# Kernel tuning notes

Measured on AMD Instinct MI355X. Metric: run time of the kernel, lower is better.

## Reference

```python
import jax, jax.numpy as jnp
import numpy as np

HID = 2048
H = 16
D_NOPE = 128
D_ROPE = 64
HEAD_DIM = D_NOPE + D_ROPE  # 192
V_DIM = 128
KV_RANK = 512
Q_RANK = 1536
THETA = 10000.0
EPS = 1e-6
B, S = 2, 2048


def _rope_cos_sin(seq_len):
    # half-dim frequencies: cos/sin have shape (seq_len, D_ROPE//2)
    inv_freq = 1.0 / (THETA ** (jnp.arange(0, D_ROPE, 2, dtype=jnp.float32) / D_ROPE))
    freqs = jnp.arange(seq_len, dtype=jnp.float32)[:, None] * inv_freq[None, :]
    return jnp.cos(freqs), jnp.sin(freqs)


def _apply_rope(x, cos, sin):
    # x: (..., D_ROPE); cos/sin broadcastable to (..., D_ROPE//2)
    half = x.shape[-1] // 2
    x1, x2 = x[..., :half], x[..., half:]
    return jnp.concatenate([x1 * cos - x2 * sin, x2 * cos + x1 * sin], axis=-1)


def _rmsnorm(x, w):
    ms = jnp.mean(jnp.square(x), axis=-1, keepdims=True)
    return x * jax.lax.rsqrt(ms + EPS) * w


def setup_inputs() -> dict:
    key = jax.random.key(0)
    ks = jax.random.split(key, 7)
    std = 0.02
    return {
        "x": jax.random.normal(ks[0], (B, S, HID), dtype=jnp.float32),
        "w_q_down": jax.random.normal(ks[1], (HID, Q_RANK), dtype=jnp.float32) * std,
        "w_q_up": jax.random.normal(ks[2], (Q_RANK, H * HEAD_DIM), dtype=jnp.float32) * std,
        "w_kv_down": jax.random.normal(ks[3], (HID, KV_RANK + D_ROPE), dtype=jnp.float32) * std,
        "kv_norm_w": jnp.ones((KV_RANK,), dtype=jnp.float32),
        "w_kv_up": jax.random.normal(ks[4], (KV_RANK, H * (D_NOPE + V_DIM)), dtype=jnp.float32) * std,
        "w_out": jax.random.normal(ks[5], (H * V_DIM, HID), dtype=jnp.float32) * std,
    }


def reference(x, w_q_down, w_q_up, w_kv_down, kv_norm_w, w_kv_up, w_out):
    b, s, _ = x.shape
    scale = 1.0 / np.sqrt(HEAD_DIM)

    # query: low-rank down then up, split into nope/rope parts
    q = (x @ w_q_down) @ w_q_up                      # (b, s, H*HEAD_DIM)
    q = q.reshape(b, s, H, HEAD_DIM)
    q_nope, q_rope = q[..., :D_NOPE], q[..., D_NOPE:]

    # KV: compressed latent + rope key component
    kv_full = x @ w_kv_down                          # (b, s, KV_RANK + D_ROPE)
    kv_c, k_rope = kv_full[..., :KV_RANK], kv_full[..., KV_RANK:]
    kv_c = _rmsnorm(kv_c, kv_norm_w)

    kv_exp = (kv_c @ w_kv_up).reshape(b, s, H, D_NOPE + V_DIM)
    k_nope, v = kv_exp[..., :D_NOPE], kv_exp[..., D_NOPE:]

    # RoPE (no past_kv -> q_offset = 0, kv_len = s)
    cos, sin = _rope_cos_sin(s)                      # (s, D_ROPE//2)
    cos4, sin4 = cos[None, :, None, :], sin[None, :, None, :]
    q_rope = _apply_rope(q_rope, cos4, sin4)         # (b, s, H, D_ROPE)
    k_rope = _apply_rope(k_rope, cos[None], sin[None])  # (b, s, D_ROPE)

    k_rope_h = jnp.broadcast_to(k_rope[:, :, None, :], (b, s, H, D_ROPE))
    k = jnp.concatenate([k_nope, k_rope_h], axis=-1)     # (b, s, H, HEAD_DIM)
    q_full = jnp.concatenate([q_nope, q_rope], axis=-1)  # (b, s, H, HEAD_DIM)

    # causal SDPA
    scores = jnp.einsum("bqhd,bkhd->bhqk", q_full, k) * scale
    causal = jnp.tril(jnp.ones((s, s), dtype=bool))
    scores = jnp.where(causal[None, None], scores, jnp.finfo(scores.dtype).min)
    attn = jax.nn.softmax(scores, axis=-1)
    out = jnp.einsum("bhqk,bkhd->bqhd", attn, v)     # (b, s, H, V_DIM)
    out = out.reshape(b, s, H * V_DIM)
    return out @ w_out
```

## Files before the change

### kernel.cpp

```cpp
#include <hip/hip_runtime.h>
#include <hip/hip_bf16.h>
#include <math.h>

#define HID    2048
#define NH     16
#define D_NOPE 128
#define D_ROPE 64
#define HD     192
#define V_DIM  128
#define KV_RANK 512
#define Q_RANK  1536
#define BATCH  2
#define SEQ    2048
#define ROWS   (BATCH*SEQ)

typedef __attribute__((ext_vector_type(8))) short short8;
typedef __attribute__((ext_vector_type(4))) float f32x4;

__device__ __forceinline__ unsigned short f2bf(float x) {
    unsigned int u = __float_as_uint(x);
    unsigned int r = (u + 0x7fffu + ((u >> 16) & 1u)) >> 16;
    return (unsigned short)r;
}
__device__ __forceinline__ float bf2f(unsigned short u) {
    return __uint_as_float((unsigned int)u << 16);
}

typedef const __attribute__((address_space(1))) unsigned int gu32;
typedef __attribute__((address_space(3))) unsigned int lu32;
__device__ __forceinline__ void gl_lds16(const void* g, void* l) {
    __builtin_amdgcn_global_load_lds((gu32*)g, (lu32*)l, 16, 0, 0);
}

template<int CTRL>
__device__ __forceinline__ float dpp_mv(float x) {
    return __int_as_float(__builtin_amdgcn_update_dpp(
        __float_as_int(x), __float_as_int(x), CTRL, 0xF, 0xF, true));
}
__device__ __forceinline__ float rowmax16(float x) {
    x = fmaxf(x, dpp_mv<0xB1>(x));
    x = fmaxf(x, dpp_mv<0x4E>(x));
    x = fmaxf(x, dpp_mv<0x141>(x));
    x = fmaxf(x, dpp_mv<0x140>(x));
    return x;
}

__global__ void rope_table_kernel(float* __restrict__ table) {
    int idx = blockIdx.x * 256 + threadIdx.x;
    int pos = idx >> 6, u = idx & 63;
    int i = u & 31;
    float invf = expf((float)i * (-9.210340371976184f / 32.0f));
    float ang = (float)pos * invf;
    table[idx] = (u < 32) ? cosf(ang) : sinf(ang);
}

__global__ __launch_bounds__(256) void convert_bf16_kernel(
    const float* __restrict__ src, unsigned short* __restrict__ dst)
{
    size_t i = (size_t)(blockIdx.x * 256 + threadIdx.x) * 4;
    float4 v = *(const float4*)(src + i);
    ushort4 u;
    u.x = f2bf(v.x); u.y = f2bf(v.y); u.z = f2bf(v.z); u.w = f2bf(v.w);
    *(ushort4*)(dst + i) = u;
}

__global__ __launch_bounds__(256) void transpose_bf16_kernel(
    const float* __restrict__ src, unsigned short* __restrict__ dst, int K, int N)
{
    __shared__ float T[64][65];
    const int n0 = blockIdx.x * 64, k0 = blockIdx.y * 64;
    const int t = threadIdx.x;
    const int c4 = t & 15, r = t >> 4;
    #pragma unroll
    for (int i = 0; i < 4; i++) {
        int row = r + i * 16;
        float4 v = *(const float4*)(src + (size_t)(k0 + row) * N + n0 + c4 * 4);
        T[row][c4*4+0] = v.x; T[row][c4*4+1] = v.y;
        T[row][c4*4+2] = v.z; T[row][c4*4+3] = v.w;
    }
    __syncthreads();
    #pragma unroll
    for (int i = 0; i < 4; i++) {
        int nrow = r + i * 16;
        ushort4 u;
        u.x = f2bf(T[c4*4+0][nrow]); u.y = f2bf(T[c4*4+1][nrow]);
        u.z = f2bf(T[c4*4+2][nrow]); u.w = f2bf(T[c4*4+3][nrow]);
        *(ushort4*)(dst + (size_t)(n0 + nrow) * K + k0 + c4 * 4) = u;
    }
}

template<int BN, bool OUT_BF16>
__global__ __launch_bounds__(256) void bgemm_kernel(
    const unsigned short* __restrict__ A,
    const unsigned short* __restrict__ Bt,
    void* __restrict__ Cv,
    int M, int N, int K)
{
    constexpr int NT = BN / 32;
    constexpr int NSLAB = 8 + BN / 16;
    const int tid  = threadIdx.x;
    const int w    = tid >> 6;
    const int lane = tid & 63;
    const int n16  = lane & 15, quad = lane >> 4;
    const int m0 = blockIdx.y * 128;
    const int n0 = blockIdx.x * BN;
    const int moff = (w & 1) * 64;
    const int noff = (w >> 1) * (NT * 16);

    __shared__ unsigned short As[128 * 32];
    __shared__ unsigned short Bs[BN * 32];

    const unsigned short* gp[4];
    unsigned short* lp[4];
    int ns = 0;
    const int rl = lane >> 2, sc = lane & 3;
    for (int s = w; s < NSLAB; s += 4) {
        int kc = sc ^ (((s * 16 + rl) >> 1) & 3);
        if (s < 8) {
            gp[ns] = A + (size_t)(m0 + s * 16 + rl) * K + kc * 8;
            lp[ns] = As + s * 512;
        } else {
            int sb = s - 8;
            gp[ns] = Bt + (size_t)(n0 + sb * 16 + rl) * K + kc * 8;
            lp[ns] = Bs + sb * 512;
        }
        ns++;
    }

    const int swz = (quad ^ ((n16 >> 1) & 3)) * 8;
    int aoff[4], boff[NT];
    #pragma unroll
    for (int mt = 0; mt < 4; mt++) aoff[mt] = (moff + mt * 16 + n16) * 32 + swz;
    #pragma unroll
    for (int nt = 0; nt < NT; nt++) boff[nt] = (noff + nt * 16 + n16) * 32 + swz;

    f32x4 acc[4][NT];
    #pragma unroll
    for (int mt = 0; mt < 4; mt++)
        #pragma unroll
        for (int nt = 0; nt < NT; nt++) acc[mt][nt] = (f32x4){0.f, 0.f, 0.f, 0.f};

    for (int k0 = 0; k0 < K; k0 += 32) {
        #pragma unroll
        for (int j = 0; j < 4; j++) if (j < ns) gl_lds16(gp[j], lp[j]);
        #pragma unroll
        for (int j = 0; j < 4; j++) if (j < ns) gp[j] += 32;
        __syncthreads();

        short8 af[4], bfr[NT];
        #pragma unroll
        for (int mt = 0; mt < 4; mt++) af[mt] = *(const short8*)(As + aoff[mt]);
        #pragma unroll
        for (int nt = 0; nt < NT; nt++) bfr[nt] = *(const short8*)(Bs + boff[nt]);
        #pragma unroll
        for (int mt = 0; mt < 4; mt++)
            #pragma unroll
            for (int nt = 0; nt < NT; nt++)
                acc[mt][nt] = __builtin_amdgcn_mfma_f32_16x16x32_bf16(
                    af[mt], bfr[nt], acc[mt][nt], 0, 0, 0);
        __syncthreads();
    }

    #pragma unroll
    for (int mt = 0; mt < 4; mt++)
        #pragma unroll
        for (int nt = 0; nt < NT; nt++)
            #pragma unroll
            for (int r = 0; r < 4; r++) {
                size_t idx = (size_t)(m0 + moff + mt * 16 + quad * 4 + r) * N
                           + n0 + noff + nt * 16 + n16;
                if (OUT_BF16) ((unsigned short*)Cv)[idx] = f2bf(acc[mt][nt][r]);
                else          ((float*)Cv)[idx] = acc[mt][nt][r];
            }
}

__global__ __launch_bounds__(256) void kv_norm_rope_kernel(
    const float* __restrict__ kv_full,
    const float* __restrict__ w,
    const float* __restrict__ table,
    unsigned short* __restrict__ kv_cb,
    unsigned short* __restrict__ k_rope_b)
{
    const int row = blockIdx.x;
    const int tid = threadIdx.x;
    const float* src = kv_full + (size_t)row * 576;
    float v0 = src[tid], v1 = src[tid + 256];
    float ss = v0*v0 + v1*v1;
    #pragma unroll
    for (int off = 32; off > 0; off >>= 1) ss += __shfl_down(ss, off);
    __shared__ float red[4];
    __shared__ float msh;
    if ((tid & 63) == 0) red[tid >> 6] = ss;
    __syncthreads();
    if (tid == 0) msh = (red[0] + red[1] + red[2] + red[3]) * (1.0f / 512.0f);
    __syncthreads();
    float f = rsqrtf(msh + 1e-6f);
    kv_cb[(size_t)row * 512 + tid]       = f2bf(v0 * f * w[tid]);
    kv_cb[(size_t)row * 512 + tid + 256] = f2bf(v1 * f * w[tid + 256]);
    if (tid < 32) {
        int pos = row & (SEQ - 1);
        float c = table[pos*64 + tid], s = table[pos*64 + 32 + tid];
        float x1 = src[512 + tid], x2 = src[512 + 32 + tid];
        k_rope_b[(size_t)row * 64 + tid]      = f2bf(x1*c - x2*s);
        k_rope_b[(size_t)row * 64 + 32 + tid] = f2bf(x2*c + x1*s);
    }
}

__global__ __launch_bounds__(256) void q_rope_b_kernel(
    unsigned short* __restrict__ qb16, const float* __restrict__ table)
{
    int g = blockIdx.x * 8 + (threadIdx.x >> 5);
    int i = threadIdx.x & 31;
    int row = g >> 4, h = g & 15;
    size_t base = (size_t)row * (NH*HD) + h * HD + D_NOPE;
    int pos = row & (SEQ - 1);
    float c = table[pos*64 + i], s = table[pos*64 + 32 + i];
    float x1 = bf2f(qb16[base + i]), x2 = bf2f(qb16[base + 32 + i]);
    qb16[base + i]      = f2bf(x1*c - x2*s);
    qb16[base + 32 + i] = f2bf(x2*c + x1*s);
}

__global__ __launch_bounds__(256) void pack_vt_kernel(
    const unsigned short* __restrict__ kv_exp_b, unsigned short* __restrict__ Vmat)
{
    const int st = blockIdx.x;
    const int h  = blockIdx.y;
    const int b  = blockIdx.z;
    const int tid = threadIdx.x;
    const int s0 = st * 64;
    __shared__ float T[64][129];

    #pragma unroll
    for (int t = 0; t < 8; t++) {
        int idx = tid + t * 256;
        int tokr = idx >> 5, c4 = idx & 31;
        ushort4 u = *(const ushort4*)(kv_exp_b +
            ((size_t)(b*SEQ) + s0 + tokr) * 4096 + h*256 + 128 + c4*4);
        T[tokr][c4*4+0] = bf2f(u.x); T[tokr][c4*4+1] = bf2f(u.y);
        T[tokr][c4*4+2] = bf2f(u.z); T[tokr][c4*4+3] = bf2f(u.w);
    }
    __syncthreads();

    int d = tid >> 1, sh = (tid & 1) * 32;
    unsigned short* op = Vmat + ((size_t)((b*NH + h) * V_DIM + d)) * SEQ + s0 + sh;
    #pragma unroll
    for (int j = 0; j < 32; j += 2) {
        ushort2 u;
        u.x = f2bf(T[sh + j][d]);
        u.y = f2bf(T[sh + j + 1][d]);
        *(ushort2*)(op + j) = u;
    }
}

__global__ __launch_bounds__(256, 3) void flash_mfma_kernel(
    const unsigned short* __restrict__ qb16,
    const unsigned short* __restrict__ kv_exp_b,
    const unsigned short* __restrict__ k_rope_b,
    const unsigned short* __restrict__ Vmat,
    unsigned short* __restrict__ attnb)
{
    const int bid  = blockIdx.x;
    const int xcd  = bid & 7, slot = bid >> 3;
    const int grp  = xcd + 8 * (slot >> 5);
    const int qb   = 31 - (slot & 31);
    const int h    = grp & 15, b = grp >> 4;
    const int tid  = threadIdx.x;
    const int w    = tid >> 6;
    const int lane = tid & 63;
    const int n16  = lane & 15;
    const int quad = lane >> 4;

    const int q0 = qb * 64 + w * 16;
    const char* kNopeB = (const char*)(kv_exp_b + (size_t)b * SEQ * 4096 + h * 256);
    const char* kRopeB = (const char*)(k_rope_b + (size_t)b * SEQ * 64);
    const char* vByte  = (const char*)(Vmat + (size_t)(b*NH + h) * V_DIM * SEQ);

    __shared__ unsigned short Ks[2][6144];
    __shared__ unsigned short Vs[2][4096];
    __shared__ unsigned short Plds[4][16][40];

    const char* gK[2]; int lK[2];
    #pragma unroll
    for (int t = 0; t < 2; t++) {
        int idx = t * 256 + tid;
        int kc = idx >> 7, key = (idx >> 2) & 31, sc = idx & 3;
        int scs = sc ^ ((key >> 1) & 3);
        gK[t] = kNopeB + (size_t)key * 8192 + kc * 64 + scs * 16;
        lK[t] = idx * 16;
    }
    const char* gR; int lR;
    {
        int kc = tid >> 7, key = (tid >> 2) & 31, sc = tid & 3;
        int scs = sc ^ ((key >> 1) & 3);
        gR = kRopeB + (size_t)key * 128 + kc * 64 + scs * 16;
        lR = (512 + tid) * 16;
    }
    const char* gV[2]; int lV[2];
    #pragma unroll
    for (int t = 0; t < 2; t++) {
        int idx = t * 256 + tid;
        int d = idx >> 2, sc = idx & 3;
        int scs = sc ^ ((d >> 1) & 3);
        gV[t] = vByte + (size_t)d * (SEQ * 2) + scs * 16;
        lV[t] = idx * 16;
    }

    auto stage = [&](int kt, int bufsel) {
        const size_t koff = (size_t)kt * 32;
        #pragma unroll
        for (int t = 0; t < 2; t++)
            gl_lds16(gK[t] + koff * 8192, (char*)Ks[bufsel] + lK[t]);
        gl_lds16(gR + koff * 128, (char*)Ks[bufsel] + lR);
        #pragma unroll
        for (int t = 0; t < 2; t++)
            gl_lds16(gV[t] + koff * 2, (char*)Vs[bufsel] + lV[t]);
    };

    short8 qf[6];
    {
        const unsigned short* qp = qb16 + ((size_t)(b*SEQ) + q0 + n16) * (NH*HD)
                                 + h * HD + quad * 8;
        #pragma unroll
        for (int kc = 0; kc < 6; kc++)
            qf[kc] = *(const short8*)(qp + kc * 32);
    }

    short8 onesf;
    #pragma unroll
    for (int j = 0; j < 8; j++) onesf[j] = (short)0x3F80;

    f32x4 O[9];
    #pragma unroll
    for (int c = 0; c < 9; c++) O[c] = (f32x4){0.f, 0.f, 0.f, 0.f};
    float mrow[4] = {-INFINITY, -INFINITY, -INFINITY, -INFINITY};

    const float scale = 0.07216878364870322f;
    const int swz = (quad ^ ((n16 >> 1) & 3)) * 8;
    const int ntB = 2 * qb + 2;

    stage(0, 0);
    int cur = 0;
    for (int kt = 0; kt < ntB; kt++) {
        __syncthreads();
        if (kt + 1 < ntB) stage(kt + 1, cur ^ 1);
        const int k0 = kt * 32;

        if (k0 <= q0 + 15) {
            const unsigned short* KsB = Ks[cur];
            const unsigned short* VsB = Vs[cur];

            f32x4 S[2];
            __builtin_amdgcn_s_setprio(1);
            #pragma unroll
            for (int half = 0; half < 2; half++) {
                f32x4 acc = (f32x4){0.f, 0.f, 0.f, 0.f};
                const int keyoff = (half * 16 + n16) * 32 + swz;
                #pragma unroll
                for (int kc = 0; kc < 6; kc++) {
                    short8 kf = *(const short8*)(KsB + kc * 1024 + keyoff);
                    acc = __builtin_amdgcn_mfma_f32_16x16x32_bf16(qf[kc], kf, acc, 0, 0, 0);
                }
                S[half] = acc;
            }
            __builtin_amdgcn_s_setprio(0);

            float p0[4], p1[4], tmax[4];
            float growth = -INFINITY;
            #pragma unroll
            for (int r = 0; r < 4; r++) {
                int row = q0 + quad*4 + r;
                float s0v = (k0 + n16      <= row) ? S[0][r] * scale : -INFINITY;
                float s1v = (k0 + 16 + n16 <= row) ? S[1][r] * scale : -INFINITY;
                p0[r] = s0v; p1[r] = s1v;
                tmax[r] = rowmax16(fmaxf(s0v, s1v));
                growth = fmaxf(growth, tmax[r] - mrow[r]);
            }
            if (!__all(growth <= 6.0f)) {
                #pragma unroll
                for (int r = 0; r < 4; r++) {
                    float mnew = fmaxf(mrow[r], tmax[r]);
                    float alpha = __expf(mrow[r] - mnew);
                    mrow[r] = mnew;
                    #pragma unroll
                    for (int c = 0; c < 9; c++) O[c][r] *= alpha;
                }
            }
            #pragma unroll
            for (int r = 0; r < 4; r++) {
                float e0 = __expf(p0[r] - mrow[r]);
                float e1 = __expf(p1[r] - mrow[r]);
                unsigned short* pw = &Plds[w][quad*4 + r][0];
                pw[n16]      = f2bf(e0);
                pw[16 + n16] = f2bf(e1);
            }

            short8 pf = *(const short8*)(&Plds[w][n16][quad * 8]);
            __builtin_amdgcn_s_setprio(1);
            #pragma unroll
            for (int c = 0; c < 8; c++) {
                short8 vf = *(const short8*)(VsB + (c * 16 + n16) * 32 + swz);
                O[c] = __builtin_amdgcn_mfma_f32_16x16x32_bf16(pf, vf, O[c], 0, 0, 0);
            }
            O[8] = __builtin_amdgcn_mfma_f32_16x16x32_bf16(pf, onesf, O[8], 0, 0, 0);
            __builtin_amdgcn_s_setprio(0);
        }
        cur ^= 1;
    }

    float invl[4];
    #pragma unroll
    for (int r = 0; r < 4; r++) invl[r] = 1.0f / O[8][r];
    #pragma unroll
    for (int c = 0; c < 8; c++) {
        #pragma unroll
        for (int r = 0; r < 4; r++) {
            size_t tok = (size_t)b * SEQ + q0 + quad*4 + r;
            attnb[tok * (NH*V_DIM) + h * V_DIM + c*16 + n16] = f2bf(O[c][r] * invl[r]);
        }
    }
}

extern "C" void kernel_launch(void* const* d_in, const int* in_sizes, int n_in,
                              void* d_out, int out_size, void* d_ws, size_t ws_size,
                              hipStream_t stream)
{
    const float* x         = (const float*)d_in[0];
    const float* w_q_down  = (const float*)d_in[1];
    const float* w_q_up    = (const float*)d_in[2];
    const float* w_kv_down = (const float*)d_in[3];
    const float* kv_norm_w = (const float*)d_in[4];
    const float* w_kv_up   = (const float*)d_in[5];
    const float* w_out     = (const float*)d_in[6];
    float* out = (float*)d_out;
    float* ws  = (float*)d_ws;

    float*          table    = ws;
    unsigned short* xb       = (unsigned short*)(ws + 131072);
    unsigned short* qdb      = (unsigned short*)(ws + 4325376);
    unsigned short* qb16     = (unsigned short*)(ws + 7471104);
    float*          kv_full  = ws + 13762560;
    unsigned short* kv_cb    = (unsigned short*)(ws + 16121856);
    unsigned short* k_rope_b = (unsigned short*)(ws + 17170432);
    unsigned short* kv_exp_b = (unsigned short*)(ws + 17301504);
    unsigned short* Vmat     = (unsigned short*)(ws + 25690112);
    unsigned short* attnb    = (unsigned short*)(ws + 29884416);
    unsigned short* wt1      = (unsigned short*)(ws + 34078720);
    unsigned short* wt2      = (unsigned short*)(ws + 35651584);
    unsigned short* wt3      = (unsigned short*)(ws + 38010880);
    unsigned short* wt4      = (unsigned short*)(ws + 38600704);
    unsigned short* wt5      = (unsigned short*)(ws + 39649280);

    rope_table_kernel<<<512, 256, 0, stream>>>(table);

    convert_bf16_kernel<<<ROWS*HID/1024, 256, 0, stream>>>(x, xb);
    transpose_bf16_kernel<<<dim3(1536/64, 2048/64), 256, 0, stream>>>(w_q_down, wt1, 2048, 1536);
    transpose_bf16_kernel<<<dim3(3072/64, 1536/64), 256, 0, stream>>>(w_q_up,   wt2, 1536, 3072);
    transpose_bf16_kernel<<<dim3(576/64,  2048/64), 256, 0, stream>>>(w_kv_down,wt3, 2048, 576);
    transpose_bf16_kernel<<<dim3(4096/64,  512/64), 256, 0, stream>>>(w_kv_up,  wt4, 512, 4096);
    transpose_bf16_kernel<<<dim3(2048/64, 2048/64), 256, 0, stream>>>(w_out,    wt5, 2048, 2048);

    bgemm_kernel<128, true><<<dim3(1536/128, ROWS/128), 256, 0, stream>>>(xb,  wt1, qdb,  ROWS, 1536, 2048);
    bgemm_kernel<128, true><<<dim3(3072/128, ROWS/128), 256, 0, stream>>>(qdb, wt2, qb16, ROWS, 3072, 1536);
    q_rope_b_kernel<<<8192, 256, 0, stream>>>(qb16, table);

    bgemm_kernel<64, false><<<dim3(576/64, ROWS/128), 256, 0, stream>>>(xb, wt3, kv_full, ROWS, 576, 2048);
    kv_norm_rope_kernel<<<ROWS, 256, 0, stream>>>(kv_full, kv_norm_w, table, kv_cb, k_rope_b);
    bgemm_kernel<128, true><<<dim3(4096/128, ROWS/128), 256, 0, stream>>>(kv_cb, wt4, kv_exp_b, ROWS, 4096, 512);
    pack_vt_kernel<<<dim3(SEQ/64, NH, BATCH), 256, 0, stream>>>(kv_exp_b, Vmat);

    flash_mfma_kernel<<<dim3(1024), 256, 0, stream>>>(qb16, kv_exp_b, k_rope_b, Vmat, attnb);

    bgemm_kernel<128, false><<<dim3(2048/128, ROWS/128), 256, 0, stream>>>(attnb, wt5, out, ROWS, 2048, 2048);
}
```

Measured before the change: 489.7 us.

## Process two 16-row query tiles per wave in flash attention to reuse K/V

Each wave now handles 32 query rows as two 16-row MFMA tiles, so each block covers 128 queries and the grid halves. Every K/V fragment loaded from LDS feeds two MFMAs, which halves K/V staging traffic per query. The causal mask is applied only on the diagonal tile, and the softmax switches to exp2 with the scale folded into the exponent and a raw-score rescale threshold. The cost is higher register pressure (occupancy hint dropped from 3 to 2), fewer blocks to fill the device, and coarser causal load balance.

```diff
diff --git a/kernel.cpp b/kernel.cpp
--- a/kernel.cpp
+++ b/kernel.cpp
@@ -252,7 +252,7 @@
     }
 }
 
-__global__ __launch_bounds__(256, 3) void flash_mfma_kernel(
+__global__ __launch_bounds__(256, 2) void flash_mfma_kernel(
     const unsigned short* __restrict__ qb16,
     const unsigned short* __restrict__ kv_exp_b,
     const unsigned short* __restrict__ k_rope_b,
@@ -261,8 +261,8 @@
 {
     const int bid  = blockIdx.x;
     const int xcd  = bid & 7, slot = bid >> 3;
-    const int grp  = xcd + 8 * (slot >> 5);
-    const int qb   = 31 - (slot & 31);
+    const int grp  = xcd + 8 * (slot >> 4);
+    const int qb   = 15 - (slot & 15);
     const int h    = grp & 15, b = grp >> 4;
     const int tid  = threadIdx.x;
     const int w    = tid >> 6;
@@ -270,14 +270,14 @@
     const int n16  = lane & 15;
     const int quad = lane >> 4;
 
-    const int q0 = qb * 64 + w * 16;
+    const int q0 = qb * 128 + w * 32;
     const char* kNopeB = (const char*)(kv_exp_b + (size_t)b * SEQ * 4096 + h * 256);
     const char* kRopeB = (const char*)(k_rope_b + (size_t)b * SEQ * 64);
     const char* vByte  = (const char*)(Vmat + (size_t)(b*NH + h) * V_DIM * SEQ);
 
     __shared__ unsigned short Ks[2][6144];
     __shared__ unsigned short Vs[2][4096];
-    __shared__ unsigned short Plds[4][16][40];
+    __shared__ unsigned short Plds[4][2][16][40];
 
     const char* gK[2]; int lK[2];
     #pragma unroll
@@ -316,27 +316,35 @@
             gl_lds16(gV[t] + koff * 2, (char*)Vs[bufsel] + lV[t]);
     };
 
-    short8 qf[6];
+    short8 qf0[6], qf1[6];
     {
-        const unsigned short* qp = qb16 + ((size_t)(b*SEQ) + q0 + n16) * (NH*HD)
-                                 + h * HD + quad * 8;
-        #pragma unroll
-        for (int kc = 0; kc < 6; kc++)
-            qf[kc] = *(const short8*)(qp + kc * 32);
+        const unsigned short* qp0 = qb16 + ((size_t)(b*SEQ) + q0 + n16) * (NH*HD)
+                                  + h * HD + quad * 8;
+        const unsigned short* qp1 = qp0 + (size_t)16 * (NH*HD);
+        #pragma unroll
+        for (int kc = 0; kc < 6; kc++) {
+            qf0[kc] = *(const short8*)(qp0 + kc * 32);
+            qf1[kc] = *(const short8*)(qp1 + kc * 32);
+        }
     }
 
     short8 onesf;
     #pragma unroll
     for (int j = 0; j < 8; j++) onesf[j] = (short)0x3F80;
 
-    f32x4 O[9];
-    #pragma unroll
-    for (int c = 0; c < 9; c++) O[c] = (f32x4){0.f, 0.f, 0.f, 0.f};
-    float mrow[4] = {-INFINITY, -INFINITY, -INFINITY, -INFINITY};
-
-    const float scale = 0.07216878364870322f;
+    f32x4 O0[9], O1[9];
+    #pragma unroll
+    for (int c = 0; c < 9; c++) {
+        O0[c] = (f32x4){0.f, 0.f, 0.f, 0.f};
+        O1[c] = (f32x4){0.f, 0.f, 0.f, 0.f};
+    }
+    float mrow0[4] = {-INFINITY, -INFINITY, -INFINITY, -INFINITY};
+    float mrow1[4] = {-INFINITY, -INFINITY, -INFINITY, -INFINITY};
+
+    const float SCLOG2 = 0.10412779736150104f;
+    const float THRRAW = 83.0f;
     const int swz = (quad ^ ((n16 >> 1) & 3)) * 8;
-    const int ntB = 2 * qb + 2;
+    const int ntB = 4 * qb + 4;
 
     stage(0, 0);
     int cur = 0;
@@ -345,77 +353,111 @@
         if (kt + 1 < ntB) stage(kt + 1, cur ^ 1);
         const int k0 = kt * 32;
 
-        if (k0 <= q0 + 15) {
+        if (k0 <= q0 + 31) {
             const unsigned short* KsB = Ks[cur];
             const unsigned short* VsB = Vs[cur];
 
-            f32x4 S[2];
+            f32x4 S0[2], S1[2];
             __builtin_amdgcn_s_setprio(1);
             #pragma unroll
             for (int half = 0; half < 2; half++) {
-                f32x4 acc = (f32x4){0.f, 0.f, 0.f, 0.f};
+                f32x4 a0 = (f32x4){0.f, 0.f, 0.f, 0.f};
+                f32x4 a1 = (f32x4){0.f, 0.f, 0.f, 0.f};
                 const int keyoff = (half * 16 + n16) * 32 + swz;
                 #pragma unroll
                 for (int kc = 0; kc < 6; kc++) {
                     short8 kf = *(const short8*)(KsB + kc * 1024 + keyoff);
-                    acc = __builtin_amdgcn_mfma_f32_16x16x32_bf16(qf[kc], kf, acc, 0, 0, 0);
+                    a0 = __builtin_amdgcn_mfma_f32_16x16x32_bf16(qf0[kc], kf, a0, 0, 0, 0);
+                    a1 = __builtin_amdgcn_mfma_f32_16x16x32_bf16(qf1[kc], kf, a1, 0, 0, 0);
                 }
-                S[half] = acc;
+                S0[half] = a0; S1[half] = a1;
             }
             __builtin_amdgcn_s_setprio(0);
 
-            float p0[4], p1[4], tmax[4];
+            float p00[4], p01[4], p10[4], p11[4];
+            if (k0 == q0) {
+                #pragma unroll
+                for (int r = 0; r < 4; r++) {
+                    int row0 = q0 + quad*4 + r, row1 = row0 + 16;
+                    p00[r] = (k0 + n16      <= row0) ? S0[0][r] : -INFINITY;
+                    p01[r] = (k0 + 16 + n16 <= row0) ? S0[1][r] : -INFINITY;
+                    p10[r] = (k0 + n16      <= row1) ? S1[0][r] : -INFINITY;
+                    p11[r] = (k0 + 16 + n16 <= row1) ? S1[1][r] : -INFINITY;
+                }
+            } else {
+                #pragma unroll
+                for (int r = 0; r < 4; r++) {
+                    p00[r] = S0[0][r]; p01[r] = S0[1][r];
+                    p10[r] = S1[0][r]; p11[r] = S1[1][r];
+                }
+            }
+
+            float tmax0[4], tmax1[4];
             float growth = -INFINITY;
             #pragma unroll
             for (int r = 0; r < 4; r++) {
-                int row = q0 + quad*4 + r;
-                float s0v = (k0 + n16      <= row) ? S[0][r] * scale : -INFINITY;
-                float s1v = (k0 + 16 + n16 <= row) ? S[1][r] * scale : -INFINITY;
-                p0[r] = s0v; p1[r] = s1v;
-                tmax[r] = rowmax16(fmaxf(s0v, s1v));
-                growth = fmaxf(growth, tmax[r] - mrow[r]);
-            }
-            if (!__all(growth <= 6.0f)) {
+                tmax0[r] = rowmax16(fmaxf(p00[r], p01[r]));
+                tmax1[r] = rowmax16(fmaxf(p10[r], p11[r]));
+                growth = fmaxf(growth,
+                    fmaxf(tmax0[r] - mrow0[r], tmax1[r] - mrow1[r]));
+            }
+            if (!__all(growth <= THRRAW)) {
                 #pragma unroll
                 for (int r = 0; r < 4; r++) {
-                    float mnew = fmaxf(mrow[r], tmax[r]);
-                    float alpha = __expf(mrow[r] - mnew);
-                    mrow[r] = mnew;
+                    float mn0 = fmaxf(mrow0[r], tmax0[r]);
+                    float a0 = exp2f((mrow0[r] - mn0) * SCLOG2);
+                    mrow0[r] = mn0;
+                    float mn1 = fmaxf(mrow1[r], tmax1[r]);
+                    float a1 = exp2f((mrow1[r] - mn1) * SCLOG2);
+                    mrow1[r] = mn1;
                     #pragma unroll
-                    for (int c = 0; c < 9; c++) O[c][r] *= alpha;
+                    for (int c = 0; c < 9; c++) { O0[c][r] *= a0; O1[c][r] *= a1; }
                 }
             }
             #pragma unroll
             for (int r = 0; r < 4; r++) {
-                float e0 = __expf(p0[r] - mrow[r]);
-                float e1 = __expf(p1[r] - mrow[r]);
-                unsigned short* pw = &Plds[w][quad*4 + r][0];
-                pw[n16]      = f2bf(e0);
-                pw[16 + n16] = f2bf(e1);
-            }
-
-            short8 pf = *(const short8*)(&Plds[w][n16][quad * 8]);
+                float e00 = exp2f((p00[r] - mrow0[r]) * SCLOG2);
+                float e01 = exp2f((p01[r] - mrow0[r]) * SCLOG2);
+                float e10 = exp2f((p10[r] - mrow1[r]) * SCLOG2);
+                float e11 = exp2f((p11[r] - mrow1[r]) * SCLOG2);
+                unsigned short* pw0 = &Plds[w][0][quad*4 + r][0];
+                pw0[n16]      = f2bf(e00);
+                pw0[16 + n16] = f2bf(e01);
+                unsigned short* pw1 = &Plds[w][1][quad*4 + r][0];
+                pw1[n16]      = f2bf(e10);
+                pw1[16 + n16] = f2bf(e11);
+            }
+
+            short8 pf0 = *(const short8*)(&Plds[w][0][n16][quad * 8]);
+            short8 pf1 = *(const short8*)(&Plds[w][1][n16][quad * 8]);
             __builtin_amdgcn_s_setprio(1);
             #pragma unroll
             for (int c = 0; c < 8; c++) {
                 short8 vf = *(const short8*)(VsB + (c * 16 + n16) * 32 + swz);
-                O[c] = __builtin_amdgcn_mfma_f32_16x16x32_bf16(pf, vf, O[c], 0, 0, 0);
-            }
-            O[8] = __builtin_amdgcn_mfma_f32_16x16x32_bf16(pf, onesf, O[8], 0, 0, 0);
+                O0[c] = __builtin_amdgcn_mfma_f32_16x16x32_bf16(pf0, vf, O0[c], 0, 0, 0);
+                O1[c] = __builtin_amdgcn_mfma_f32_16x16x32_bf16(pf1, vf, O1[c], 0, 0, 0);
+            }
+            O0[8] = __builtin_amdgcn_mfma_f32_16x16x32_bf16(pf0, onesf, O0[8], 0, 0, 0);
+            O1[8] = __builtin_amdgcn_mfma_f32_16x16x32_bf16(pf1, onesf, O1[8], 0, 0, 0);
             __builtin_amdgcn_s_setprio(0);
         }
         cur ^= 1;
     }
 
-    float invl[4];
-    #pragma unroll
-    for (int r = 0; r < 4; r++) invl[r] = 1.0f / O[8][r];
+    float invl0[4], invl1[4];
+    #pragma unroll
+    for (int r = 0; r < 4; r++) {
+        invl0[r] = 1.0f / O0[8][r];
+        invl1[r] = 1.0f / O1[8][r];
+    }
     #pragma unroll
     for (int c = 0; c < 8; c++) {
         #pragma unroll
         for (int r = 0; r < 4; r++) {
-            size_t tok = (size_t)b * SEQ + q0 + quad*4 + r;
-            attnb[tok * (NH*V_DIM) + h * V_DIM + c*16 + n16] = f2bf(O[c][r] * invl[r]);
+            size_t tok0 = (size_t)b * SEQ + q0 + quad*4 + r;
+            attnb[tok0 * (NH*V_DIM) + h * V_DIM + c*16 + n16] = f2bf(O0[c][r] * invl0[r]);
+            size_t tok1 = tok0 + 16;
+            attnb[tok1 * (NH*V_DIM) + h * V_DIM + c*16 + n16] = f2bf(O1[c][r] * invl1[r]);
         }
     }
 }
@@ -468,7 +510,7 @@
     bgemm_kernel<128, true><<<dim3(4096/128, ROWS/128), 256, 0, stream>>>(kv_cb, wt4, kv_exp_b, ROWS, 4096, 512);
     pack_vt_kernel<<<dim3(SEQ/64, NH, BATCH), 256, 0, stream>>>(kv_exp_b, Vmat);
 
-    flash_mfma_kernel<<<dim3(1024), 256, 0, stream>>>(qb16, kv_exp_b, k_rope_b, Vmat, attnb);
+    flash_mfma_kernel<<<dim3(512), 256, 0, stream>>>(qb16, kv_exp_b, k_rope_b, Vmat, attnb);
 
     bgemm_kernel<128, false><<<dim3(2048/128, ROWS/128), 256, 0, stream>>>(attnb, wt5, out, ROWS, 2048, 2048);
 }
```

New measurement: 531.4 us. 8.5% more time.
